# Kernel tuning notes

Measured on AMD Instinct MI355X. Metric: run time of the kernel, lower is better.

## Reference

```python
import jax, jax.numpy as jnp
import numpy as np

NBITS = 4
GROUP_SIZE = 128


def setup_inputs() -> dict:
    key = jax.random.key(0)
    k1, k2, k3, k4, k5 = jax.random.split(key, 5)
    B, S, K, N = 2, 2048, 4096, 4096
    G = K // GROUP_SIZE  # 32 groups along K
    x = jax.random.normal(k1, (B, S, K), dtype=jnp.float16)
    # unpacked uint4 weights stored in int32 carrier, values in [0, 2^nbits)
    W_q = jax.random.randint(k2, (N, K), 0, 2 ** NBITS, dtype=jnp.int32)
    scale = (jax.random.uniform(k3, (N, G), dtype=jnp.float32) * 0.01 + 0.001).astype(jnp.float16)
    zero = (jax.random.uniform(k4, (N, G), dtype=jnp.float32) * (2 ** NBITS)).astype(jnp.float16)
    bias = jax.random.normal(k5, (N,), dtype=jnp.float16)
    return {"x": x, "W_q": W_q, "scale": scale, "zero": zero, "bias": bias}


def _dequant(W_q, scale, zero):
    # W_q: [N, K] int, scale/zero: [N, K//group_size] fp16
    # zeros_mode='original': W = (W_q - zero) * scale, per group along K
    N, K = W_q.shape
    G = K // GROUP_SIZE
    Wg = W_q.reshape(N, G, GROUP_SIZE).astype(jnp.float16)
    Wd = (Wg - zero[:, :, None]) * scale[:, :, None]
    return Wd.reshape(N, K)


def reference(x, W_q, scale, zero, bias):
    # out = x @ W_deq^T + bias   (layout 'nt': W is [N, K])
    W = _dequant(W_q, scale, zero)            # [N, K] fp16
    out = jnp.einsum('bsk,nk->bsn', x, W)     # [B, S, N] fp16 accum per module config
    return out + bias
```

## Files before the change

kernel.cpp:

```cpp
#include <hip/hip_runtime.h>
#include <hip/hip_bf16.h>


typedef __bf16 bf16x8 __attribute__((ext_vector_type(8)));
typedef float f32x4 __attribute__((ext_vector_type(4)));

#define BM 128
#define BN 128
#define BK 64

static __device__ __forceinline__ int pack_bf16x2(float a, float b) {
    __hip_bfloat162 p = __float22bfloat162_rn(make_float2(a, b));
    int r;
    __builtin_memcpy(&r, &p, 4);
    return r;
}

__global__ __launch_bounds__(256) void prepass_kernel(
    const float* __restrict__ X, unsigned short* __restrict__ Ad,
    const int*   __restrict__ Wq,
    const float* __restrict__ scale,
    const float* __restrict__ zero,
    unsigned short* __restrict__ Wd,
    int aUnits, int wUnits, int K, int G, int GROUP)
{
    const int stride = gridDim.x * blockDim.x;
    const int t0     = blockIdx.x * blockDim.x + threadIdx.x;

    for (int u = t0; u < aUnits; u += stride) {
        const long long f = (long long)u * 8;
        const float4 a0 = *(const float4*)(X + f);
        const float4 a1 = *(const float4*)(X + f + 4);
        int4 d;
        d.x = pack_bf16x2(a0.x, a0.y);
        d.y = pack_bf16x2(a0.z, a0.w);
        d.z = pack_bf16x2(a1.x, a1.y);
        d.w = pack_bf16x2(a1.z, a1.w);
        *(int4*)(Ad + f) = d;
    }

    const int unitsPerRow = K >> 3;
    for (int u = t0; u < wUnits; u += stride) {
        const int n = u / unitsPerRow;
        const int k = (u - n * unitsPerRow) * 8;
        const int g = k / GROUP;
        const float s  = scale[(long long)n * G + g];
        const float z  = zero [(long long)n * G + g];
        const float mz = -z * s;

        const long long f = (long long)n * K + k;
        const int4 q0 = *(const int4*)(Wq + f);
        const int4 q1 = *(const int4*)(Wq + f + 4);
        int4 d;
        d.x = pack_bf16x2((float)q0.x * s + mz, (float)q0.y * s + mz);
        d.y = pack_bf16x2((float)q0.z * s + mz, (float)q0.w * s + mz);
        d.z = pack_bf16x2((float)q1.x * s + mz, (float)q1.y * s + mz);
        d.w = pack_bf16x2((float)q1.z * s + mz, (float)q1.w * s + mz);
        *(int4*)(Wd + f) = d;
    }
}

__global__ __launch_bounds__(512, 2) void gemm256_8ph(
    const unsigned short* __restrict__ A,
    const unsigned short* __restrict__ Bw,
    const float* __restrict__ bias,
    float*       __restrict__ C,
    int M, int N, int K)
{
    __shared__ unsigned short ldsA[2][2][8192];
    __shared__ unsigned short ldsB[2][2][8192];

    const int tid  = threadIdx.x;
    const int lane = tid & 63;
    const int wave = tid >> 6;
    const int wm   = wave >> 2;
    const int wn   = wave & 3;

    const int nwg  = (N >> 8) * (M >> 8);
    const int cpx  = nwg >> 3;
    const int bid  = blockIdx.x;
    const int wgid = (bid & 7) * cpx + (bid >> 3);
    const int bx   = wgid % (N >> 8);
    const int by   = wgid / (N >> 8);
    const int blockN0 = bx << 8;
    const int blockM0 = by << 8;

    long long gSrcA[2], gSrcB[2];
    int ldsDst[2];
#pragma unroll
    for (int l = 0; l < 2; ++l) {
        const int s  = l * 512 + tid;
        const int R  = s >> 3;
        const int j  = s & 7;
        const int ju = j ^ (R & 7);
        const int r  = 2 * R + (ju >> 2);
        const int cc = ju & 3;
        gSrcA[l] = (long long)(blockM0 + r) * K + cc * 8;
        gSrcB[l] = (long long)(blockN0 + r) * K + cc * 8;
        ldsDst[l] = (l * 512 + wave * 64) * 8;
    }

    const int row16 = lane & 15;
    const int quad  = lane >> 4;
    int offA[8], offB[4];
#pragma unroll
    for (int m = 0; m < 8; ++m) {
        const int r = wm * 128 + m * 16 + row16;
        const int R = r >> 1;
        const int j = (((r & 1) << 2) | quad) ^ (R & 7);
        offA[m] = R * 64 + j * 8;
    }
#pragma unroll
    for (int n = 0; n < 4; ++n) {
        const int r = wn * 64 + n * 16 + row16;
        const int R = r >> 1;
        const int j = (((r & 1) << 2) | quad) ^ (R & 7);
        offB[n] = R * 64 + j * 8;
    }

    f32x4 acc[8][4];
#pragma unroll
    for (int m = 0; m < 8; ++m)
#pragma unroll
        for (int n = 0; n < 4; ++n)
            acc[m][n] = (f32x4){0.f, 0.f, 0.f, 0.f};

#define STAGE_A(T_, KH_)                                                      \
    do {                                                                      \
        const int b_ = (T_) & 1;                                              \
        const long long ko_ = (long long)(T_) * 64 + (KH_) * 32;              \
        __builtin_amdgcn_global_load_lds(                                     \
            (const __attribute__((address_space(1))) unsigned int*)           \
                (A + gSrcA[0] + ko_),                                         \
            (__attribute__((address_space(3))) unsigned int*)                 \
                (&ldsA[b_][KH_][ldsDst[0]]), 16, 0, 0);                       \
        __builtin_amdgcn_global_load_lds(                                     \
            (const __attribute__((address_space(1))) unsigned int*)           \
                (A + gSrcA[1] + ko_),                                         \
            (__attribute__((address_space(3))) unsigned int*)                 \
                (&ldsA[b_][KH_][ldsDst[1]]), 16, 0, 0);                       \
    } while (0)

#define STAGE_B(T_, KH_)                                                      \
    do {                                                                      \
        const int b_ = (T_) & 1;                                              \
        const long long ko_ = (long long)(T_) * 64 + (KH_) * 32;              \
        __builtin_amdgcn_global_load_lds(                                     \
            (const __attribute__((address_space(1))) unsigned int*)           \
                (Bw + gSrcB[0] + ko_),                                        \
            (__attribute__((address_space(3))) unsigned int*)                 \
                (&ldsB[b_][KH_][ldsDst[0]]), 16, 0, 0);                       \
        __builtin_amdgcn_global_load_lds(                                     \
            (const __attribute__((address_space(1))) unsigned int*)           \
                (Bw + gSrcB[1] + ko_),                                        \
            (__attribute__((address_space(3))) unsigned int*)                 \
                (&ldsB[b_][KH_][ldsDst[1]]), 16, 0, 0);                       \
    } while (0)

#define READ_BV(c_, kk_)                                                      \
    bv0 = *(const bf16x8*)&ldsB[c_][kk_][offB[0]];                            \
    bv1 = *(const bf16x8*)&ldsB[c_][kk_][offB[1]];                            \
    bv2 = *(const bf16x8*)&ldsB[c_][kk_][offB[2]];                            \
    bv3 = *(const bf16x8*)&ldsB[c_][kk_][offB[3]];

#define READ_AV(c_, kk_, mh_)                                                 \
    av0 = *(const bf16x8*)&ldsA[c_][kk_][offA[(mh_) * 4 + 0]];                \
    av1 = *(const bf16x8*)&ldsA[c_][kk_][offA[(mh_) * 4 + 1]];                \
    av2 = *(const bf16x8*)&ldsA[c_][kk_][offA[(mh_) * 4 + 2]];                \
    av3 = *(const bf16x8*)&ldsA[c_][kk_][offA[(mh_) * 4 + 3]];

#define MFROW(mi_, av_)                                                       \
    acc[mi_][0] = __builtin_amdgcn_mfma_f32_16x16x32_bf16(av_, bv0, acc[mi_][0], 0, 0, 0); \
    acc[mi_][1] = __builtin_amdgcn_mfma_f32_16x16x32_bf16(av_, bv1, acc[mi_][1], 0, 0, 0); \
    acc[mi_][2] = __builtin_amdgcn_mfma_f32_16x16x32_bf16(av_, bv2, acc[mi_][2], 0, 0, 0); \
    acc[mi_][3] = __builtin_amdgcn_mfma_f32_16x16x32_bf16(av_, bv3, acc[mi_][3], 0, 0, 0);

#define MFMA16(mh_)                                                           \
    __builtin_amdgcn_s_setprio(1);                                            \
    MFROW((mh_) * 4 + 0, av0);                                                \
    MFROW((mh_) * 4 + 1, av1);                                                \
    MFROW((mh_) * 4 + 2, av2);                                                \
    MFROW((mh_) * 4 + 3, av3);                                                \
    __builtin_amdgcn_s_setprio(0);

#define BAR() __builtin_amdgcn_s_barrier()

    const int NT = K >> 6;

    STAGE_A(0, 0); STAGE_B(0, 0); STAGE_A(0, 1); STAGE_B(0, 1);
    STAGE_B(1, 0); STAGE_A(1, 0);
    asm volatile("s_waitcnt vmcnt(4)" ::: "memory");
    BAR();

    bf16x8 av0, av1, av2, av3, bv0, bv1, bv2, bv3;

#pragma unroll 2
    for (int T = 0; T <= NT - 3; ++T) {
        const int c = T & 1;
        READ_BV(c, 0);
        READ_AV(c, 0, 0);
        STAGE_B(T + 1, 1);
        BAR();
        MFMA16(0);
        READ_AV(c, 0, 1);
        STAGE_A(T + 1, 1);
        BAR();
        MFMA16(1);
        READ_BV(c, 1);
        READ_AV(c, 1, 0);
        STAGE_B(T + 2, 0);
        BAR();
        MFMA16(0);
        READ_AV(c, 1, 1);
        STAGE_A(T + 2, 0);
        asm volatile("s_waitcnt vmcnt(4)" ::: "memory");
        BAR();
        MFMA16(1);
    }

    {
        const int c2 = (NT - 2) & 1;
        READ_BV(c2, 0);
        READ_AV(c2, 0, 0);
        STAGE_B(NT - 1, 1);
        BAR();
        MFMA16(0);
        READ_AV(c2, 0, 1);
        STAGE_A(NT - 1, 1);
        BAR();
        MFMA16(1);
        READ_BV(c2, 1);
        READ_AV(c2, 1, 0);
        BAR();
        MFMA16(0);
        READ_AV(c2, 1, 1);
        asm volatile("s_waitcnt vmcnt(0)" ::: "memory");
        BAR();
        MFMA16(1);
    }
    {
        const int c1 = (NT - 1) & 1;
        READ_BV(c1, 0); READ_AV(c1, 0, 0); MFMA16(0);
        READ_AV(c1, 0, 1); MFMA16(1);
        READ_BV(c1, 1); READ_AV(c1, 1, 0); MFMA16(0);
        READ_AV(c1, 1, 1); MFMA16(1);
    }

#undef STAGE_A
#undef STAGE_B
#undef READ_BV
#undef READ_AV
#undef MFROW
#undef MFMA16
#undef BAR

    const int colBase = blockN0 + wn * 64;
    const int rowBase = blockM0 + wm * 128;
    float biasf[4];
#pragma unroll
    for (int n = 0; n < 4; ++n)
        biasf[n] = bias[colBase + n * 16 + row16];

#pragma unroll
    for (int m = 0; m < 8; ++m) {
        const int row0 = rowBase + m * 16 + quad * 4;
#pragma unroll
        for (int n = 0; n < 4; ++n) {
            const int col = colBase + n * 16 + row16;
#pragma unroll
            for (int r = 0; r < 4; ++r) {
                C[(long long)(row0 + r) * N + col] = acc[m][n][r] + biasf[n];
            }
        }
    }
}

__global__ __launch_bounds__(256, 2) void gemm_bf16_nt(
    const unsigned short* __restrict__ A,
    const unsigned short* __restrict__ Bw,
    const float* __restrict__ bias,
    float*       __restrict__ C,
    int M, int N, int K)
{
    __shared__ unsigned short ldsA[BM * BK];
    __shared__ unsigned short ldsB[BN * BK];

    const int tid   = threadIdx.x;
    const int lane  = tid & 63;
    const int wave  = tid >> 6;
    const int waveM = wave >> 1;
    const int waveN = wave & 1;

    const int blockN0 = blockIdx.x * BN;
    const int blockM0 = blockIdx.y * BM;

    const long long aBase = (long long)blockM0 * K;
    const long long bBase = (long long)blockN0 * K;

    const int rowInChunk = lane >> 3;
    const int colChunkSw = (lane & 7) ^ rowInChunk;
    const int col8       = colChunkSw * 8;

    f32x4 acc[4][4];
#pragma unroll
    for (int i = 0; i < 4; ++i)
#pragma unroll
        for (int j = 0; j < 4; ++j)
            acc[i][j] = (f32x4){0.f, 0.f, 0.f, 0.f};

    const int row16 = lane & 15;
    const int quad  = lane >> 4;
    const int sw    = row16 & 7;

    for (int k0 = 0; k0 < K; k0 += BK) {
        __syncthreads();
#pragma unroll
        for (int c = 0; c < 4; ++c) {
            const int chunk = (wave << 2) | c;
            const int row   = (chunk << 3) | rowInChunk;
            const unsigned short* gA = A  + aBase + (long long)row * K + k0 + col8;
            const unsigned short* gB = Bw + bBase + (long long)row * K + k0 + col8;
            __builtin_amdgcn_global_load_lds(
                (const __attribute__((address_space(1))) unsigned int*)gA,
                (__attribute__((address_space(3))) unsigned int*)&ldsA[chunk * 512],
                16, 0, 0);
            __builtin_amdgcn_global_load_lds(
                (const __attribute__((address_space(1))) unsigned int*)gB,
                (__attribute__((address_space(3))) unsigned int*)&ldsB[chunk * 512],
                16, 0, 0);
        }
        __syncthreads();

#pragma unroll
        for (int kk = 0; kk < 2; ++kk) {
            bf16x8 av[4], bv[4];
#pragma unroll
            for (int i = 0; i < 4; ++i) {
                const int r    = waveM * 64 + i * 16 + row16;
                const int slot = (kk * 4 + quad) ^ sw;
                av[i] = *(const bf16x8*)&ldsA[r * BK + slot * 8];
            }
#pragma unroll
            for (int j = 0; j < 4; ++j) {
                const int r    = waveN * 64 + j * 16 + row16;
                const int slot = (kk * 4 + quad) ^ sw;
                bv[j] = *(const bf16x8*)&ldsB[r * BK + slot * 8];
            }
#pragma unroll
            for (int i = 0; i < 4; ++i)
#pragma unroll
                for (int j = 0; j < 4; ++j)
                    acc[i][j] = __builtin_amdgcn_mfma_f32_16x16x32_bf16(
                        av[i], bv[j], acc[i][j], 0, 0, 0);
        }
    }

    const int colBase = blockN0 + waveN * 64;
    const int rowBase = blockM0 + waveM * 64;
    float biasf[4];
#pragma unroll
    for (int j = 0; j < 4; ++j)
        biasf[j] = bias[colBase + j * 16 + row16];

#pragma unroll
    for (int i = 0; i < 4; ++i) {
        const int row0 = rowBase + i * 16 + quad * 4;
#pragma unroll
        for (int j = 0; j < 4; ++j) {
            const int col = colBase + j * 16 + row16;
#pragma unroll
            for (int r = 0; r < 4; ++r) {
                C[(long long)(row0 + r) * N + col] = acc[i][j][r] + biasf[j];
            }
        }
    }
}

__global__ __launch_bounds__(256) void hqq_gemm_fused_f32(
    const float* __restrict__ A,
    const int*   __restrict__ Wq,
    const float* __restrict__ scale,
    const float* __restrict__ zero,
    const float* __restrict__ bias,
    float*       __restrict__ C,
    int M, int N, int K, int G, int GROUP)
{
    __shared__ unsigned short ldsA[BM * BK];
    __shared__ unsigned short ldsB[BN * BK];

    const int tid   = threadIdx.x;
    const int lane  = tid & 63;
    const int wave  = tid >> 6;
    const int waveM = wave >> 1;
    const int waveN = wave & 1;

    const int blockN0 = blockIdx.x * BN;
    const int blockM0 = blockIdx.y * BM;

    const int row16 = lane & 15;
    const int quad  = lane >> 4;

    f32x4 acc[4][4];
#pragma unroll
    for (int i = 0; i < 4; ++i)
#pragma unroll
        for (int j = 0; j < 4; ++j)
            acc[i][j] = (f32x4){0.f, 0.f, 0.f, 0.f};

    for (int k0 = 0; k0 < K; k0 += BK) {
        const int g = k0 / GROUP;
        int4 ra[4], rb[4];
#pragma unroll
        for (int c = 0; c < 4; ++c) {
            const int chunk = c * 256 + tid;
            const int row   = chunk >> 3;
            const int col   = (chunk & 7) * 8;

            const float* ap = A + (long long)(blockM0 + row) * K + k0 + col;
            const float4 a0 = *(const float4*)(ap);
            const float4 a1 = *(const float4*)(ap + 4);
            int4 da;
            da.x = pack_bf16x2(a0.x, a0.y);
            da.y = pack_bf16x2(a0.z, a0.w);
            da.z = pack_bf16x2(a1.x, a1.y);
            da.w = pack_bf16x2(a1.z, a1.w);
            ra[c] = da;

            const int n = blockN0 + row;
            const float s  = scale[(long long)n * G + g];
            const float z  = zero [(long long)n * G + g];
            const float mz = -z * s;
            const long long wb = (long long)n * K + k0 + col;
            const int4 q0 = *(const int4*)(Wq + wb);
            const int4 q1 = *(const int4*)(Wq + wb + 4);
            int4 db;
            db.x = pack_bf16x2((float)q0.x * s + mz, (float)q0.y * s + mz);
            db.y = pack_bf16x2((float)q0.z * s + mz, (float)q0.w * s + mz);
            db.z = pack_bf16x2((float)q1.x * s + mz, (float)q1.y * s + mz);
            db.w = pack_bf16x2((float)q1.z * s + mz, (float)q1.w * s + mz);
            rb[c] = db;
        }

        __syncthreads();
#pragma unroll
        for (int c = 0; c < 4; ++c) {
            const int chunk = c * 256 + tid;
            *(int4*)&ldsA[chunk * 8] = ra[c];
            *(int4*)&ldsB[chunk * 8] = rb[c];
        }
        __syncthreads();

#pragma unroll
        for (int kk = 0; kk < 2; ++kk) {
            const int kOff = kk * 32 + quad * 8;
            bf16x8 av[4], bv[4];
#pragma unroll
            for (int i = 0; i < 4; ++i)
                av[i] = *(const bf16x8*)&ldsA[(waveM * 64 + i * 16 + row16) * BK + kOff];
#pragma unroll
            for (int j = 0; j < 4; ++j)
                bv[j] = *(const bf16x8*)&ldsB[(waveN * 64 + j * 16 + row16) * BK + kOff];
#pragma unroll
            for (int i = 0; i < 4; ++i)
#pragma unroll
                for (int j = 0; j < 4; ++j)
                    acc[i][j] = __builtin_amdgcn_mfma_f32_16x16x32_bf16(
                        av[i], bv[j], acc[i][j], 0, 0, 0);
        }
    }

    const int colBase = blockN0 + waveN * 64;
    const int rowBase = blockM0 + waveM * 64;
    float biasf[4];
#pragma unroll
    for (int j = 0; j < 4; ++j)
        biasf[j] = bias[colBase + j * 16 + row16];

#pragma unroll
    for (int i = 0; i < 4; ++i) {
        const int row0 = rowBase + i * 16 + quad * 4;
#pragma unroll
        for (int j = 0; j < 4; ++j) {
            const int col = colBase + j * 16 + row16;
#pragma unroll
            for (int r = 0; r < 4; ++r) {
                C[(long long)(row0 + r) * N + col] = acc[i][j][r] + biasf[j];
            }
        }
    }
}

extern "C" void kernel_launch(void* const* d_in, const int* in_sizes, int n_in,
                              void* d_out, int out_size, void* d_ws, size_t ws_size,
                              hipStream_t stream) {
    (void)n_in; (void)out_size;

    const float* x     = (const float*)d_in[0];
    const int*   Wq    = (const int*)d_in[1];
    const float* scale = (const float*)d_in[2];
    const float* zero  = (const float*)d_in[3];
    const float* bias  = (const float*)d_in[4];
    float*       out   = (float*)d_out;

    const int N     = in_sizes[4];
    const int G     = in_sizes[2] / N;
    const int K     = in_sizes[1] / N;
    const int M     = in_sizes[0] / K;
    const int GROUP = K / G;

    const size_t needWs = (size_t)N * K * 2 + (size_t)M * K * 2;

    if (ws_size >= needWs) {
        unsigned short* Wd = (unsigned short*)d_ws;
        unsigned short* Ad = (unsigned short*)((char*)d_ws + (size_t)N * K * 2);

        const int aUnits = (int)((long long)M * K / 8);
        const int wUnits = (int)((long long)N * K / 8);
        prepass_kernel<<<2048, 256, 0, stream>>>(x, Ad, Wq, scale, zero, Wd,
                                                 aUnits, wUnits, K, G, GROUP);

        const int nwg = (N >> 8) * (M >> 8);
        const int NT  = K >> 6;
        if ((M % 256) == 0 && (N % 256) == 0 && (K % 64) == 0 && NT >= 4 &&
            (nwg % 8) == 0) {
            gemm256_8ph<<<nwg, 512, 0, stream>>>(Ad, Wd, bias, out, M, N, K);
        } else {
            dim3 grid(N / BN, M / BM);
            gemm_bf16_nt<<<grid, 256, 0, stream>>>(Ad, Wd, bias, out, M, N, K);
        }
    } else {
        dim3 grid(N / BN, M / BM);
        hqq_gemm_fused_f32<<<grid, 256, 0, stream>>>(x, Wq, scale, zero, bias, out,
                                                     M, N, K, G, GROUP);
    }
}
```

Before: 288.1 us.

## Software-pipeline LDS fragment reads one phase ahead of MFMA in GEMM loop

Restructures the 8-phase main loop so the LDS reads for the next phase (A halves, B halves) are issued before the current phase's MFMA block, using double fragment registers (ax/ay, bv/bw). This is meant to hide LDS read latency behind matrix math instead of stalling before each MFMA group. Barriers now follow explicit lgkmcnt(0) waits, and the global-load wait count changes from vmcnt(4) to vmcnt(2). The extra fragment registers raise VGPR pressure under a launch bound of 2 blocks per CU, and the altered wait counts risk races or extra stalls.

```diff
diff --git a/kernel.cpp b/kernel.cpp
--- a/kernel.cpp
+++ b/kernel.cpp
@@ -60,7 +60,7 @@
     }
 }
 
-__global__ __launch_bounds__(512, 2) void gemm256_8ph(
+__global__ __launch_bounds__(512, 2) void gemm256_hoist(
     const unsigned short* __restrict__ A,
     const unsigned short* __restrict__ Bw,
     const float* __restrict__ bias,
@@ -157,33 +157,54 @@
                 (&ldsB[b_][KH_][ldsDst[1]]), 16, 0, 0);                       \
     } while (0)
 
-#define READ_BV(c_, kk_)                                                      \
-    bv0 = *(const bf16x8*)&ldsB[c_][kk_][offB[0]];                            \
-    bv1 = *(const bf16x8*)&ldsB[c_][kk_][offB[1]];                            \
-    bv2 = *(const bf16x8*)&ldsB[c_][kk_][offB[2]];                            \
-    bv3 = *(const bf16x8*)&ldsB[c_][kk_][offB[3]];
-
-#define READ_AV(c_, kk_, mh_)                                                 \
-    av0 = *(const bf16x8*)&ldsA[c_][kk_][offA[(mh_) * 4 + 0]];                \
-    av1 = *(const bf16x8*)&ldsA[c_][kk_][offA[(mh_) * 4 + 1]];                \
-    av2 = *(const bf16x8*)&ldsA[c_][kk_][offA[(mh_) * 4 + 2]];                \
-    av3 = *(const bf16x8*)&ldsA[c_][kk_][offA[(mh_) * 4 + 3]];
-
-#define MFROW(mi_, av_)                                                       \
-    acc[mi_][0] = __builtin_amdgcn_mfma_f32_16x16x32_bf16(av_, bv0, acc[mi_][0], 0, 0, 0); \
-    acc[mi_][1] = __builtin_amdgcn_mfma_f32_16x16x32_bf16(av_, bv1, acc[mi_][1], 0, 0, 0); \
-    acc[mi_][2] = __builtin_amdgcn_mfma_f32_16x16x32_bf16(av_, bv2, acc[mi_][2], 0, 0, 0); \
-    acc[mi_][3] = __builtin_amdgcn_mfma_f32_16x16x32_bf16(av_, bv3, acc[mi_][3], 0, 0, 0);
-
-#define MFMA16(mh_)                                                           \
+#define READ_BV(c_)                                                           \
+    bv0 = *(const bf16x8*)&ldsB[c_][0][offB[0]];                              \
+    bv1 = *(const bf16x8*)&ldsB[c_][0][offB[1]];                              \
+    bv2 = *(const bf16x8*)&ldsB[c_][0][offB[2]];                              \
+    bv3 = *(const bf16x8*)&ldsB[c_][0][offB[3]];
+
+#define READ_BW(c_)                                                           \
+    bw0 = *(const bf16x8*)&ldsB[c_][1][offB[0]];                              \
+    bw1 = *(const bf16x8*)&ldsB[c_][1][offB[1]];                              \
+    bw2 = *(const bf16x8*)&ldsB[c_][1][offB[2]];                              \
+    bw3 = *(const bf16x8*)&ldsB[c_][1][offB[3]];
+
+#define READ_AX(c_, kh_)                                                      \
+    ax0 = *(const bf16x8*)&ldsA[c_][kh_][offA[0]];                            \
+    ax1 = *(const bf16x8*)&ldsA[c_][kh_][offA[1]];                            \
+    ax2 = *(const bf16x8*)&ldsA[c_][kh_][offA[2]];                            \
+    ax3 = *(const bf16x8*)&ldsA[c_][kh_][offA[3]];
+
+#define READ_AY(c_, kh_)                                                      \
+    ay0 = *(const bf16x8*)&ldsA[c_][kh_][offA[4]];                            \
+    ay1 = *(const bf16x8*)&ldsA[c_][kh_][offA[5]];                            \
+    ay2 = *(const bf16x8*)&ldsA[c_][kh_][offA[6]];                            \
+    ay3 = *(const bf16x8*)&ldsA[c_][kh_][offA[7]];
+
+#define MFROW4(mi_, av_, b0_, b1_, b2_, b3_)                                  \
+    acc[mi_][0] = __builtin_amdgcn_mfma_f32_16x16x32_bf16(av_, b0_, acc[mi_][0], 0, 0, 0); \
+    acc[mi_][1] = __builtin_amdgcn_mfma_f32_16x16x32_bf16(av_, b1_, acc[mi_][1], 0, 0, 0); \
+    acc[mi_][2] = __builtin_amdgcn_mfma_f32_16x16x32_bf16(av_, b2_, acc[mi_][2], 0, 0, 0); \
+    acc[mi_][3] = __builtin_amdgcn_mfma_f32_16x16x32_bf16(av_, b3_, acc[mi_][3], 0, 0, 0);
+
+#define MF16_X(b0_, b1_, b2_, b3_)                      \
     __builtin_amdgcn_s_setprio(1);                                            \
-    MFROW((mh_) * 4 + 0, av0);                                                \
-    MFROW((mh_) * 4 + 1, av1);                                                \
-    MFROW((mh_) * 4 + 2, av2);                                                \
-    MFROW((mh_) * 4 + 3, av3);                                                \
+    MFROW4(0, ax0, b0_, b1_, b2_, b3_);                                       \
+    MFROW4(1, ax1, b0_, b1_, b2_, b3_);                                       \
+    MFROW4(2, ax2, b0_, b1_, b2_, b3_);                                       \
+    MFROW4(3, ax3, b0_, b1_, b2_, b3_);                                       \
     __builtin_amdgcn_s_setprio(0);
 
-#define BAR() __builtin_amdgcn_s_barrier()
+#define MF16_Y(b0_, b1_, b2_, b3_)                      \
+    __builtin_amdgcn_s_setprio(1);                                            \
+    MFROW4(4, ay0, b0_, b1_, b2_, b3_);                                       \
+    MFROW4(5, ay1, b0_, b1_, b2_, b3_);                                       \
+    MFROW4(6, ay2, b0_, b1_, b2_, b3_);                                       \
+    MFROW4(7, ay3, b0_, b1_, b2_, b3_);                                       \
+    __builtin_amdgcn_s_setprio(0);
+
+#define LGKM0() asm volatile("s_waitcnt lgkmcnt(0)" ::: "memory")
+#define BAR()   __builtin_amdgcn_s_barrier()
 
     const int NT = K >> 6;
 
@@ -192,66 +213,75 @@
     asm volatile("s_waitcnt vmcnt(4)" ::: "memory");
     BAR();
 
-    bf16x8 av0, av1, av2, av3, bv0, bv1, bv2, bv3;
+    bf16x8 bv0, bv1, bv2, bv3, bw0, bw1, bw2, bw3;
+    bf16x8 ax0, ax1, ax2, ax3, ay0, ay1, ay2, ay3;
+
+    READ_BV(0);
+    READ_AX(0, 0);
 
 #pragma unroll 2
     for (int T = 0; T <= NT - 3; ++T) {
-        const int c = T & 1;
-        READ_BV(c, 0);
-        READ_AV(c, 0, 0);
+        const int c = T & 1, cn = c ^ 1;
+        LGKM0(); BAR();
         STAGE_B(T + 1, 1);
+        READ_AY(c, 0);
+        MF16_X(bv0, bv1, bv2, bv3);
+        LGKM0(); BAR();
+        STAGE_A(T + 1, 1);
+        READ_BW(c);
+        READ_AX(c, 1);
+        MF16_Y(bv0, bv1, bv2, bv3);
+        LGKM0(); BAR();
+        STAGE_B(T + 2, 0);
+        READ_AY(c, 1);
+        MF16_X(bw0, bw1, bw2, bw3);
+        LGKM0();
+        asm volatile("s_waitcnt vmcnt(2)" ::: "memory");
         BAR();
-        MFMA16(0);
-        READ_AV(c, 0, 1);
-        STAGE_A(T + 1, 1);
-        BAR();
-        MFMA16(1);
-        READ_BV(c, 1);
-        READ_AV(c, 1, 0);
-        STAGE_B(T + 2, 0);
-        BAR();
-        MFMA16(0);
-        READ_AV(c, 1, 1);
         STAGE_A(T + 2, 0);
-        asm volatile("s_waitcnt vmcnt(4)" ::: "memory");
-        BAR();
-        MFMA16(1);
+        READ_BV(cn);
+        READ_AX(cn, 0);
+        MF16_Y(bw0, bw1, bw2, bw3);
     }
 
     {
-        const int c2 = (NT - 2) & 1;
-        READ_BV(c2, 0);
-        READ_AV(c2, 0, 0);
+        const int cE = (NT - 2) & 1, cL = (NT - 1) & 1;
+        LGKM0(); BAR();
         STAGE_B(NT - 1, 1);
-        BAR();
-        MFMA16(0);
-        READ_AV(c2, 0, 1);
+        READ_AY(cE, 0);
+        MF16_X(bv0, bv1, bv2, bv3);
+        LGKM0(); BAR();
         STAGE_A(NT - 1, 1);
-        BAR();
-        MFMA16(1);
-        READ_BV(c2, 1);
-        READ_AV(c2, 1, 0);
-        BAR();
-        MFMA16(0);
-        READ_AV(c2, 1, 1);
+        READ_BW(cE);
+        READ_AX(cE, 1);
+        MF16_Y(bv0, bv1, bv2, bv3);
+        READ_AY(cE, 1);
+        MF16_X(bw0, bw1, bw2, bw3);
         asm volatile("s_waitcnt vmcnt(0)" ::: "memory");
         BAR();
-        MFMA16(1);
-    }
-    {
-        const int c1 = (NT - 1) & 1;
-        READ_BV(c1, 0); READ_AV(c1, 0, 0); MFMA16(0);
-        READ_AV(c1, 0, 1); MFMA16(1);
-        READ_BV(c1, 1); READ_AV(c1, 1, 0); MFMA16(0);
-        READ_AV(c1, 1, 1); MFMA16(1);
+        READ_BV(cL);
+        READ_AX(cL, 0);
+        MF16_Y(bw0, bw1, bw2, bw3);
+        READ_AY(cL, 0);
+        MF16_X(bv0, bv1, bv2, bv3);
+        READ_BW(cL);
+        READ_AX(cL, 1);
+        MF16_Y(bv0, bv1, bv2, bv3);
+        READ_AY(cL, 1);
+        MF16_X(bw0, bw1, bw2, bw3);
+        MF16_Y(bw0, bw1, bw2, bw3);
     }
 
 #undef STAGE_A
 #undef STAGE_B
 #undef READ_BV
-#undef READ_AV
-#undef MFROW
-#undef MFMA16
+#undef READ_BW
+#undef READ_AX
+#undef READ_AY
+#undef MFROW4
+#undef MF16_X
+#undef MF16_Y
+#undef LGKM0
 #undef BAR
 
     const int colBase = blockN0 + wn * 64;
@@ -523,7 +553,7 @@
         const int NT  = K >> 6;
         if ((M % 256) == 0 && (N % 256) == 0 && (K % 64) == 0 && NT >= 4 &&
             (nwg % 8) == 0) {
-            gemm256_8ph<<<nwg, 512, 0, stream>>>(Ad, Wd, bias, out, M, N, K);
+            gemm256_hoist<<<nwg, 512, 0, stream>>>(Ad, Wd, bias, out, M, N, K);
         } else {
             dim3 grid(N / BN, M / BM);
             gemm_bf16_nt<<<grid, 256, 0, stream>>>(Ad, Wd, bias, out, M, N, K);
```

Result: slower. 305.8 us (+6.1%).
